# Kernel tuning notes

Hardware: AMD Instinct MI355X
Metric: run time of the kernel (lower is better)

## Reference

```python
import jax, jax.numpy as jnp
import numpy as np

VOCAB = 50257
EMBED = 512
HEADS = 8
HEAD_DIM = EMBED // HEADS
WINDOW = 128
NUM_CLASS = 20
B, S = 4, 2048


def setup_inputs() -> dict:
    key = jax.random.key(0)
    ks = jax.random.split(key, 16)
    sc = 0.02
    inp = {
        'text': jax.random.randint(ks[0], (B, S), 0, VOCAB),
        'emb': jax.random.normal(ks[1], (VOCAB, EMBED), jnp.float32) * sc,
        'in_w': jax.random.normal(ks[2], (3 * EMBED, EMBED), jnp.float32) * sc,
        'in_b': jnp.zeros((3 * EMBED,), jnp.float32),
        'out_w': jax.random.normal(ks[3], (EMBED, EMBED), jnp.float32) * sc,
        'out_b': jnp.zeros((EMBED,), jnp.float32),
        'w1': jax.random.normal(ks[4], (512, EMBED), jnp.float32) * sc,
        'b1': jnp.zeros((512,), jnp.float32),
        'w2': jax.random.normal(ks[5], (256, 512), jnp.float32) * sc,
        'b2': jnp.zeros((256,), jnp.float32),
        'w3': jax.random.normal(ks[6], (128, 256), jnp.float32) * sc,
        'b3': jnp.zeros((128,), jnp.float32),
        'w4': jax.random.normal(ks[7], (NUM_CLASS, 128), jnp.float32) * sc,
        'b4': jnp.zeros((NUM_CLASS,), jnp.float32),
    }
    return inp


def _banded_mask(seq_len, window):
    i = jnp.arange(seq_len)[:, None]
    j = jnp.arange(seq_len)[None, :]
    allowed = jnp.abs(i - j) <= window  # band of width 2*window+1
    return jnp.where(allowed, 0.0, -jnp.inf).astype(jnp.float32)


def reference(text, emb, in_w, in_b, out_w, out_b, w1, b1, w2, b2, w3, b3, w4, b4):
    # Embedding lookup (dropout is identity in eval mode)
    x = emb[text]  # [B, S, E]
    b, s, e = x.shape

    # torch nn.MultiheadAttention: packed in_proj, scaling by 1/sqrt(head_dim)
    wq, wk, wv = in_w[:e], in_w[e:2 * e], in_w[2 * e:]
    bq, bk, bv = in_b[:e], in_b[e:2 * e], in_b[2 * e:]
    q = (x @ wq.T + bq).reshape(b, s, HEADS, HEAD_DIM)
    k = (x @ wk.T + bk).reshape(b, s, HEADS, HEAD_DIM)
    v = (x @ wv.T + bv).reshape(b, s, HEADS, HEAD_DIM)

    mask = _banded_mask(s, WINDOW)  # [S, S] additive, -inf outside band
    scores = jnp.einsum('bihd,bjhd->bhij', q, k) / jnp.sqrt(jnp.float32(HEAD_DIM))
    probs = jax.nn.softmax(scores + mask, axis=-1)  # [B, H, S, S]
    attn = jnp.einsum('bhij,bjhd->bihd', probs, v).reshape(b, s, e)
    attn = attn @ out_w.T + out_b  # [B, S, E]

    # max-pool over sequence
    ctx = jnp.max(attn, axis=1)  # [B, E]

    # MLP head with leaky_relu (negative_slope=0.01, torch default)
    h = jax.nn.leaky_relu(ctx @ w1.T + b1, 0.01)
    h = jax.nn.leaky_relu(h @ w2.T + b2, 0.01)
    h = jax.nn.leaky_relu(h @ w3.T + b3, 0.01)
    return h @ w4.T + b4  # [B, NUM_CLASS]
```

## Files before the change

kernel.cpp:

```cpp
#include <hip/hip_runtime.h>

typedef unsigned short u16;
typedef __attribute__((ext_vector_type(8))) short bf16x8;
typedef __attribute__((ext_vector_type(4))) float f32x4;

#define S_LEN 2048
#define EMBED 512
#define HEADS 8
#define HDIM 64
#define BATCH 4
#define TOKENS (BATCH * S_LEN)

__device__ __forceinline__ u16 f2bf(float f) {
  union { float f; unsigned u; } v;
  v.f = f;
  unsigned r = v.u + 0x7fffu + ((v.u >> 16) & 1u);
  return (u16)(r >> 16);
}

__device__ __forceinline__ void gl2lds16(const void* g, void* l) {
  __builtin_amdgcn_global_load_lds(
      (const __attribute__((address_space(1))) void*)g,
      (__attribute__((address_space(3))) void*)l, 16, 0, 0);
}

__global__ __launch_bounds__(256) void gather_kernel(
    const int* __restrict__ text, const float* __restrict__ emb,
    u16* __restrict__ Xb) {
  const int t = blockIdx.x;
  const int tid = threadIdx.x;
  const size_t src = (size_t)text[t] * EMBED + tid * 2;
  const float2 v = *(const float2*)(emb + src);
  u16* dst = Xb + (size_t)t * EMBED + tid * 2;
  dst[0] = f2bf(v.x);
  dst[1] = f2bf(v.y);
}

__global__ __launch_bounds__(256) void convw_kernel(
    const float* __restrict__ in_w, const float* __restrict__ out_w,
    u16* __restrict__ Wq, u16* __restrict__ Wo) {
  const int idx4 = (blockIdx.x * 256 + threadIdx.x) * 4;
  const float* src;
  u16* dst;
  if (idx4 < 1536 * 512) { src = in_w + idx4; dst = Wq + idx4; }
  else { src = out_w + (idx4 - 1536 * 512); dst = Wo + (idx4 - 1536 * 512); }
  const float4 v = *(const float4*)src;
  dst[0] = f2bf(v.x); dst[1] = f2bf(v.y); dst[2] = f2bf(v.z); dst[3] = f2bf(v.w);
}

__global__ __launch_bounds__(256, 3) void qkv_mfma(
    const u16* __restrict__ Xb, const u16* __restrict__ Wq,
    const float* __restrict__ in_b,
    u16* __restrict__ qg, u16* __restrict__ kg, u16* __restrict__ vt) {
  __shared__ u16 As[128 * 64];
  __shared__ u16 Bs[128 * 64];
  const int m0 = blockIdx.x * 128, n0 = blockIdx.y * 128;
  const int tid = threadIdx.x;
  const int w = tid >> 6, l = tid & 63, quad = l >> 4, ln = l & 15;
  const int rb = (w >> 1) * 64, cb = (w & 1) * 64;

  f32x4 acc[4][4] = {};

  for (int k0 = 0; k0 < EMBED; k0 += 64) {
#pragma unroll
    for (int it = 0; it < 4; ++it) {
      const int chunk = it * 256 + tid;
      const int row = chunk >> 3, cp = chunk & 7, c = cp ^ (row & 7);
      gl2lds16(Xb + (size_t)(m0 + row) * EMBED + k0 + c * 8, &As[chunk * 8]);
      gl2lds16(Wq + (size_t)(n0 + row) * EMBED + k0 + c * 8, &Bs[chunk * 8]);
    }
    __syncthreads();
#pragma unroll
    for (int s = 0; s < 2; ++s) {
      bf16x8 af[4], bf[4];
#pragma unroll
      for (int i = 0; i < 4; ++i) {
        const int r = rb + 16 * i + ln;
        af[i] = *(const bf16x8*)&As[r * 64 + (((s << 2) + quad) ^ (r & 7)) * 8];
      }
#pragma unroll
      for (int j = 0; j < 4; ++j) {
        const int n = cb + 16 * j + ln;
        bf[j] = *(const bf16x8*)&Bs[n * 64 + (((s << 2) + quad) ^ (n & 7)) * 8];
      }
#pragma unroll
      for (int i = 0; i < 4; ++i)
#pragma unroll
        for (int j = 0; j < 4; ++j)
          acc[i][j] = __builtin_amdgcn_mfma_f32_16x16x32_bf16(af[i], bf[j], acc[i][j], 0, 0, 0);
    }
    __syncthreads();
  }

#pragma unroll
  for (int j = 0; j < 4; ++j) {
    const int n = n0 + cb + 16 * j + ln;
    const float bias = in_b[n];
    const int sec = n >> 9, f = n & 511, h = f >> 6, d = f & 63;
#pragma unroll
    for (int i = 0; i < 4; ++i) {
#pragma unroll
      for (int r = 0; r < 4; ++r) {
        const int t = m0 + rb + 16 * i + quad * 4 + r;
        const int b = t >> 11, s = t & 2047;
        const float val = acc[i][j][r] + bias;
        if (sec == 0)
          qg[((size_t)((b * HEADS + h) * S_LEN + s)) * HDIM + d] = f2bf(val * 0.125f);
        else if (sec == 1)
          kg[((size_t)((b * HEADS + h) * S_LEN + s)) * HDIM + d] = f2bf(val);
        else
          vt[((size_t)((b * HEADS + h) * HDIM + d)) * S_LEN + s] = f2bf(val);
      }
    }
  }
}

__global__ __launch_bounds__(256, 3) void attn_mfma(
    const u16* __restrict__ qg, const u16* __restrict__ kg,
    const u16* __restrict__ vt, u16* __restrict__ attnb) {
  __shared__ u16 KV[320 * 64];
  __shared__ u16 Pb[4][16 * 40];
  const int bh = blockIdx.y;
  const int i0 = blockIdx.x * 64;
  const int jb = i0 - 128;
  const int tid = threadIdx.x;
  const int w = tid >> 6, l = tid & 63, quad = l >> 4, ln = l & 15;

  const u16* qrow = qg + ((size_t)bh * S_LEN + i0 + w * 16 + ln) * HDIM;
  bf16x8 qf[2];
  qf[0] = *(const bf16x8*)(qrow + quad * 8);
  qf[1] = *(const bf16x8*)(qrow + 32 + quad * 8);

  const u16* kbase = kg + (size_t)bh * S_LEN * HDIM;
#pragma unroll
  for (int it = 0; it < 10; ++it) {
    const int chunk = it * 256 + tid;
    const int row = chunk >> 3, cp = chunk & 7, c = cp ^ (row & 7);
    int gj = jb + row;
    gj = gj < 0 ? 0 : (gj > S_LEN - 1 ? S_LEN - 1 : gj);
    gl2lds16(kbase + (size_t)gj * HDIM + c * 8, &KV[chunk * 8]);
  }
  __syncthreads();

  f32x4 sc[20];
#pragma unroll
  for (int jt = 0; jt < 20; ++jt) {
    const int r = jt * 16 + ln;
    const bf16x8 b0 = *(const bf16x8*)&KV[r * 64 + ((quad) ^ (r & 7)) * 8];
    const bf16x8 b1 = *(const bf16x8*)&KV[r * 64 + ((4 + quad) ^ (r & 7)) * 8];
    f32x4 a = {};
    a = __builtin_amdgcn_mfma_f32_16x16x32_bf16(qf[0], b0, a, 0, 0, 0);
    a = __builtin_amdgcn_mfma_f32_16x16x32_bf16(qf[1], b1, a, 0, 0, 0);
    sc[jt] = a;
  }
  __syncthreads();

  const u16* vbase = vt + (size_t)bh * HDIM * S_LEN;
#pragma unroll
  for (int it = 0; it < 10; ++it) {
    const int chunk = it * 256 + tid;
    const int row = chunk / 40, cp = chunk % 40, c = cp ^ (row & 7);
    int gc = jb + c * 8;
    gc = gc < 0 ? 0 : (gc > S_LEN - 8 ? S_LEN - 8 : gc);
    gl2lds16(vbase + (size_t)row * S_LEN + gc, &KV[chunk * 8]);
  }

  const int gibase = i0 + w * 16 + quad * 4;
  float mrow[4] = {-1e30f, -1e30f, -1e30f, -1e30f}, lrow[4];
#pragma unroll
  for (int jt = 0; jt < 20; ++jt) {
    const int gj = jb + jt * 16 + ln;
#pragma unroll
    for (int r = 0; r < 4; ++r) {
      const int dij = (gibase + r) - gj;
      const bool valid = (gj >= 0) && (gj < S_LEN) && (dij <= 128) && (dij >= -128);
      const float v = valid ? sc[jt][r] : -1e30f;
      sc[jt][r] = v;
      mrow[r] = fmaxf(mrow[r], v);
    }
  }
#pragma unroll
  for (int r = 0; r < 4; ++r) {
    mrow[r] = fmaxf(mrow[r], __shfl_xor(mrow[r], 1));
    mrow[r] = fmaxf(mrow[r], __shfl_xor(mrow[r], 2));
    mrow[r] = fmaxf(mrow[r], __shfl_xor(mrow[r], 4));
    mrow[r] = fmaxf(mrow[r], __shfl_xor(mrow[r], 8));
    lrow[r] = 0.f;
  }
#pragma unroll
  for (int jt = 0; jt < 20; ++jt)
#pragma unroll
    for (int r = 0; r < 4; ++r) {
      const float e = __expf(sc[jt][r] - mrow[r]);
      sc[jt][r] = e;
      lrow[r] += e;
    }
#pragma unroll
  for (int r = 0; r < 4; ++r) {
    lrow[r] += __shfl_xor(lrow[r], 1);
    lrow[r] += __shfl_xor(lrow[r], 2);
    lrow[r] += __shfl_xor(lrow[r], 4);
    lrow[r] += __shfl_xor(lrow[r], 8);
    lrow[r] = 1.0f / lrow[r];
  }
#pragma unroll
  for (int jt = 0; jt < 20; ++jt)
#pragma unroll
    for (int r = 0; r < 4; ++r) sc[jt][r] *= lrow[r];

  __syncthreads();

  f32x4 oacc[4] = {};
  u16* pb = &Pb[w][0];
#pragma unroll
  for (int kt = 0; kt < 10; ++kt) {
#pragma unroll
    for (int tt = 0; tt < 2; ++tt) {
      const int jt = kt * 2 + tt;
#pragma unroll
      for (int r = 0; r < 4; ++r)
        pb[(quad * 4 + r) * 40 + ln + 16 * tt] = f2bf(sc[jt][r]);
    }
    __asm__ volatile("" ::: "memory");
    const bf16x8 pa = *(const bf16x8*)&pb[ln * 40 + quad * 8];
#pragma unroll
    for (int dt = 0; dt < 4; ++dt) {
      const int d = dt * 16 + ln;
      const bf16x8 vb = *(const bf16x8*)&KV[d * 320 + ((kt * 4 + quad) ^ (d & 7)) * 8];
      oacc[dt] = __builtin_amdgcn_mfma_f32_16x16x32_bf16(pa, vb, oacc[dt], 0, 0, 0);
    }
  }

  const int b = bh >> 3, h = bh & 7;
#pragma unroll
  for (int dt = 0; dt < 4; ++dt) {
    const int d = h * HDIM + dt * 16 + ln;
#pragma unroll
    for (int r = 0; r < 4; ++r) {
      const int gi = i0 + w * 16 + quad * 4 + r;
      attnb[((size_t)(b * S_LEN + gi)) * EMBED + d] = f2bf(oacc[dt][r]);
    }
  }
}

__global__ __launch_bounds__(256, 3) void outproj_mfma(
    const u16* __restrict__ attnb, const u16* __restrict__ Wo,
    const float* __restrict__ out_b, float* __restrict__ pmax) {
  __shared__ u16 As[128 * 64];
  __shared__ u16 Bs[128 * 64];
  __shared__ float red[4][64];
  const int m0 = blockIdx.x * 128, n0 = blockIdx.y * 128;
  const int tid = threadIdx.x;
  const int w = tid >> 6, l = tid & 63, quad = l >> 4, ln = l & 15;
  const int rb = (w >> 1) * 64, cb = (w & 1) * 64;

  f32x4 acc[4][4] = {};

  for (int k0 = 0; k0 < EMBED; k0 += 64) {
#pragma unroll
    for (int it = 0; it < 4; ++it) {
      const int chunk = it * 256 + tid;
      const int row = chunk >> 3, cp = chunk & 7, c = cp ^ (row & 7);
      gl2lds16(attnb + (size_t)(m0 + row) * EMBED + k0 + c * 8, &As[chunk * 8]);
      gl2lds16(Wo + (size_t)(n0 + row) * EMBED + k0 + c * 8, &Bs[chunk * 8]);
    }
    __syncthreads();
#pragma unroll
    for (int s = 0; s < 2; ++s) {
      bf16x8 af[4], bf[4];
#pragma unroll
      for (int i = 0; i < 4; ++i) {
        const int r = rb + 16 * i + ln;
        af[i] = *(const bf16x8*)&As[r * 64 + (((s << 2) + quad) ^ (r & 7)) * 8];
      }
#pragma unroll
      for (int j = 0; j < 4; ++j) {
        const int n = cb + 16 * j + ln;
        bf[j] = *(const bf16x8*)&Bs[n * 64 + (((s << 2) + quad) ^ (n & 7)) * 8];
      }
#pragma unroll
      for (int i = 0; i < 4; ++i)
#pragma unroll
        for (int j = 0; j < 4; ++j)
          acc[i][j] = __builtin_amdgcn_mfma_f32_16x16x32_bf16(af[i], bf[j], acc[i][j], 0, 0, 0);
    }
    __syncthreads();
  }

  float cm[4];
#pragma unroll
  for (int j = 0; j < 4; ++j) {
    float m = -1e30f;
#pragma unroll
    for (int i = 0; i < 4; ++i)
#pragma unroll
      for (int r = 0; r < 4; ++r) m = fmaxf(m, acc[i][j][r]);
    m = fmaxf(m, __shfl_xor(m, 16));
    m = fmaxf(m, __shfl_xor(m, 32));
    cm[j] = m;
  }
  if (l < 16) {
#pragma unroll
    for (int j = 0; j < 4; ++j) red[w][ln + 16 * j] = cm[j];
  }
  __syncthreads();
  if (tid < 128) {
    const int ch = tid >> 6, cw = tid & 63;
    const float m = fmaxf(red[ch][cw], red[ch + 2][cw]);
    const int n = n0 + ch * 64 + cw;
    const int b = m0 >> 11, stile = (m0 >> 7) & 15;
    pmax[(size_t)(b * 16 + stile) * EMBED + n] = m + out_b[n];
  }
}

__global__ __launch_bounds__(256) void mlp_ctx_l1(
    const float* __restrict__ pmax, const float* __restrict__ w1,
    const float* __restrict__ b1, float* __restrict__ h1g) {
  __shared__ float ctx[512];
  const int b = blockIdx.x >> 3, chunk = blockIdx.x & 7;
  const int tid = threadIdx.x;

  for (int e = tid; e < 512; e += 256) {
    float m = -1e30f;
#pragma unroll
    for (int t = 0; t < 16; ++t) m = fmaxf(m, pmax[(size_t)(b * 16 + t) * 512 + e]);
    ctx[e] = m;
  }
  __syncthreads();

  const int o = chunk * 64 + (tid >> 2), kq = tid & 3;
  float acc = 0.f;
  const float* wr = w1 + (size_t)o * 512 + kq * 128;
  const float* xr = ctx + kq * 128;
  for (int k = 0; k < 128; k += 4) {
    const float4 wv = *(const float4*)(wr + k);
    const float4 xv = *(const float4*)(xr + k);
    acc += wv.x * xv.x + wv.y * xv.y + wv.z * xv.z + wv.w * xv.w;
  }
  acc += __shfl_xor(acc, 1);
  acc += __shfl_xor(acc, 2);
  if (kq == 0) {
    const float a = acc + b1[o];
    h1g[b * 512 + o] = a > 0.f ? a : 0.01f * a;
  }
}

__global__ __launch_bounds__(256) void mlp_l2(
    const float* __restrict__ h1g, const float* __restrict__ w2,
    const float* __restrict__ b2, float* __restrict__ h2g) {
  __shared__ float xb[512];
  const int b = blockIdx.x >> 2, chunk = blockIdx.x & 3;
  const int tid = threadIdx.x;
  for (int e = tid; e < 512; e += 256) xb[e] = h1g[b * 512 + e];
  __syncthreads();

  const int o = chunk * 64 + (tid >> 2), kq = tid & 3;
  float acc = 0.f;
  const float* wr = w2 + (size_t)o * 512 + kq * 128;
  const float* xr = xb + kq * 128;
  for (int k = 0; k < 128; k += 4) {
    const float4 wv = *(const float4*)(wr + k);
    const float4 xv = *(const float4*)(xr + k);
    acc += wv.x * xv.x + wv.y * xv.y + wv.z * xv.z + wv.w * xv.w;
  }
  acc += __shfl_xor(acc, 1);
  acc += __shfl_xor(acc, 2);
  if (kq == 0) {
    const float a = acc + b2[o];
    h2g[b * 256 + o] = a > 0.f ? a : 0.01f * a;
  }
}

__global__ __launch_bounds__(256) void mlp_l34(
    const float* __restrict__ h2g,
    const float* __restrict__ w3, const float* __restrict__ b3,
    const float* __restrict__ w4, const float* __restrict__ b4,
    float* __restrict__ out) {
  __shared__ float xb[256], h3[128];
  const int b = blockIdx.x, tid = threadIdx.x;
  if (tid < 256) xb[tid] = h2g[b * 256 + tid];
  __syncthreads();

  {
    const int o = tid >> 1, kh = tid & 1;
    float acc = 0.f;
    const float* wr = w3 + (size_t)o * 256 + kh * 128;
    const float* xr = xb + kh * 128;
    for (int k = 0; k < 128; k += 4) {
      const float4 wv = *(const float4*)(wr + k);
      const float4 xv = *(const float4*)(xr + k);
      acc += wv.x * xv.x + wv.y * xv.y + wv.z * xv.z + wv.w * xv.w;
    }
    acc += __shfl_xor(acc, 1);
    if (kh == 0) { const float a = acc + b3[o]; h3[o] = a > 0.f ? a : 0.01f * a; }
  }
  __syncthreads();

  if (tid < 160) {
    const int o = tid >> 3, ks = tid & 7;
    const float* wr = w4 + (size_t)o * 128 + ks * 16;
    const float* xr = h3 + ks * 16;
    float acc = 0.f;
    for (int k = 0; k < 16; k += 4) {
      const float4 wv = *(const float4*)(wr + k);
      const float4 xv = *(const float4*)(xr + k);
      acc += wv.x * xv.x + wv.y * xv.y + wv.z * xv.z + wv.w * xv.w;
    }
    acc += __shfl_xor(acc, 1);
    acc += __shfl_xor(acc, 2);
    acc += __shfl_xor(acc, 4);
    if (ks == 0) out[b * 20 + o] = acc + b4[o];
  }
}

extern "C" void kernel_launch(void* const* d_in, const int* in_sizes, int n_in,
                              void* d_out, int out_size, void* d_ws, size_t ws_size,
                              hipStream_t stream) {
  (void)in_sizes; (void)n_in; (void)out_size; (void)ws_size;
  const int*   text  = (const int*)d_in[0];
  const float* emb   = (const float*)d_in[1];
  const float* in_w  = (const float*)d_in[2];
  const float* in_b  = (const float*)d_in[3];
  const float* out_w = (const float*)d_in[4];
  const float* out_b = (const float*)d_in[5];
  const float* w1 = (const float*)d_in[6];
  const float* b1 = (const float*)d_in[7];
  const float* w2 = (const float*)d_in[8];
  const float* b2 = (const float*)d_in[9];
  const float* w3 = (const float*)d_in[10];
  const float* b3 = (const float*)d_in[11];
  const float* w4 = (const float*)d_in[12];
  const float* b4 = (const float*)d_in[13];

  char* ws = (char*)d_ws;
  u16* Xb   = (u16*)(ws);
  u16* Wq   = (u16*)(ws + 8388608);
  u16* Wo   = (u16*)(ws + 9961472);
  u16* qg   = (u16*)(ws + 10485760);
  u16* kg   = (u16*)(ws + 18874368);
  u16* vt   = (u16*)(ws + 27262976);
  u16* attn = (u16*)(ws + 35651584);
  float* pmax = (float*)(ws + 44040192);
  float* h1g  = (float*)(ws + 44171264);
  float* h2g  = (float*)(ws + 44179456);

  gather_kernel<<<TOKENS, 256, 0, stream>>>(text, emb, Xb);
  convw_kernel<<<1024, 256, 0, stream>>>(in_w, out_w, Wq, Wo);
  qkv_mfma<<<dim3(64, 12), 256, 0, stream>>>(Xb, Wq, in_b, qg, kg, vt);
  attn_mfma<<<dim3(32, 32), 256, 0, stream>>>(qg, kg, vt, attn);
  outproj_mfma<<<dim3(64, 4), 256, 0, stream>>>(attn, Wo, out_b, pmax);
  mlp_ctx_l1<<<32, 256, 0, stream>>>(pmax, w1, b1, h1g);
  mlp_l2<<<16, 256, 0, stream>>>(h1g, w2, b2, h2g);
  mlp_l34<<<4, 256, 0, stream>>>(h2g, w3, b3, w4, b4, (float*)d_out);
}
```

Measured before the change: 240.5 us.

## Fuse prep kernels, skip out-of-band attention tiles, swap grid order, pack stores

Merges the embedding gather and the weight bf16 conversion into one kernel that uses 8-wide vector loads and stores. In the attention kernel, each wave now computes only the key tiles that overlap its band, skipping the rest in the QK, softmax and PV loops. P is staged through a full swizzled LDS buffer instead of a per-wave bounce buffer, which doubles LDS use and lowers launch bounds to 2 blocks per CU. GEMM grids are transposed so consecutive blocks share the same row tile, and V-transpose stores are packed in pairs.

```diff
diff --git a/kernel.cpp b/kernel.cpp
--- a/kernel.cpp
+++ b/kernel.cpp
@@ -24,28 +24,31 @@
       (__attribute__((address_space(3))) void*)l, 16, 0, 0);
 }
 
-__global__ __launch_bounds__(256) void gather_kernel(
+__global__ __launch_bounds__(256) void prep_kernel(
     const int* __restrict__ text, const float* __restrict__ emb,
-    u16* __restrict__ Xb) {
-  const int t = blockIdx.x;
-  const int tid = threadIdx.x;
-  const size_t src = (size_t)text[t] * EMBED + tid * 2;
-  const float2 v = *(const float2*)(emb + src);
-  u16* dst = Xb + (size_t)t * EMBED + tid * 2;
-  dst[0] = f2bf(v.x);
-  dst[1] = f2bf(v.y);
-}
-
-__global__ __launch_bounds__(256) void convw_kernel(
     const float* __restrict__ in_w, const float* __restrict__ out_w,
-    u16* __restrict__ Wq, u16* __restrict__ Wo) {
-  const int idx4 = (blockIdx.x * 256 + threadIdx.x) * 4;
+    u16* __restrict__ Xb, u16* __restrict__ Wq, u16* __restrict__ Wo) {
+  const int bid = blockIdx.x;
+  const int idx = bid * 256 + threadIdx.x;
   const float* src;
   u16* dst;
-  if (idx4 < 1536 * 512) { src = in_w + idx4; dst = Wq + idx4; }
-  else { src = out_w + (idx4 - 1536 * 512); dst = Wo + (idx4 - 1536 * 512); }
-  const float4 v = *(const float4*)src;
-  dst[0] = f2bf(v.x); dst[1] = f2bf(v.y); dst[2] = f2bf(v.z); dst[3] = f2bf(v.w);
+  if (bid < 2048) {
+    const int t = idx >> 6, c8 = (idx & 63) * 8;
+    src = emb + (size_t)text[t] * EMBED + c8;
+    dst = Xb + (size_t)t * EMBED + c8;
+  } else {
+    const int w8 = (idx - 2048 * 256) * 8;
+    if (w8 < 1536 * 512) { src = in_w + w8; dst = Wq + w8; }
+    else { src = out_w + (w8 - 1536 * 512); dst = Wo + (w8 - 1536 * 512); }
+  }
+  const float4 a = *(const float4*)src;
+  const float4 b = *(const float4*)(src + 4);
+  uint4 p;
+  p.x = (unsigned)f2bf(a.x) | ((unsigned)f2bf(a.y) << 16);
+  p.y = (unsigned)f2bf(a.z) | ((unsigned)f2bf(a.w) << 16);
+  p.z = (unsigned)f2bf(b.x) | ((unsigned)f2bf(b.y) << 16);
+  p.w = (unsigned)f2bf(b.z) | ((unsigned)f2bf(b.w) << 16);
+  *(uint4*)dst = p;
 }
 
 __global__ __launch_bounds__(256, 3) void qkv_mfma(
@@ -54,7 +57,7 @@
     u16* __restrict__ qg, u16* __restrict__ kg, u16* __restrict__ vt) {
   __shared__ u16 As[128 * 64];
   __shared__ u16 Bs[128 * 64];
-  const int m0 = blockIdx.x * 128, n0 = blockIdx.y * 128;
+  const int m0 = blockIdx.y * 128, n0 = blockIdx.x * 128;
   const int tid = threadIdx.x;
   const int w = tid >> 6, l = tid & 63, quad = l >> 4, ln = l & 15;
   const int rb = (w >> 1) * 64, cb = (w & 1) * 64;
@@ -99,32 +102,47 @@
     const int sec = n >> 9, f = n & 511, h = f >> 6, d = f & 63;
 #pragma unroll
     for (int i = 0; i < 4; ++i) {
-#pragma unroll
-      for (int r = 0; r < 4; ++r) {
-        const int t = m0 + rb + 16 * i + quad * 4 + r;
-        const int b = t >> 11, s = t & 2047;
-        const float val = acc[i][j][r] + bias;
-        if (sec == 0)
-          qg[((size_t)((b * HEADS + h) * S_LEN + s)) * HDIM + d] = f2bf(val * 0.125f);
-        else if (sec == 1)
-          kg[((size_t)((b * HEADS + h) * S_LEN + s)) * HDIM + d] = f2bf(val);
-        else
-          vt[((size_t)((b * HEADS + h) * HDIM + d)) * S_LEN + s] = f2bf(val);
+      if (sec == 2) {
+#pragma unroll
+        for (int r = 0; r < 4; r += 2) {
+          const int t = m0 + rb + 16 * i + quad * 4 + r;
+          const int b = t >> 11, s = t & 2047;
+          const unsigned p = (unsigned)f2bf(acc[i][j][r] + bias) |
+                             ((unsigned)f2bf(acc[i][j][r + 1] + bias) << 16);
+          *(unsigned*)&vt[((size_t)((b * HEADS + h) * HDIM + d)) * S_LEN + s] = p;
+        }
+      } else {
+#pragma unroll
+        for (int r = 0; r < 4; ++r) {
+          const int t = m0 + rb + 16 * i + quad * 4 + r;
+          const int b = t >> 11, s = t & 2047;
+          const float val = acc[i][j][r] + bias;
+          if (sec == 0)
+            qg[((size_t)((b * HEADS + h) * S_LEN + s)) * HDIM + d] = f2bf(val * 0.125f);
+          else
+            kg[((size_t)((b * HEADS + h) * S_LEN + s)) * HDIM + d] = f2bf(val);
+        }
       }
     }
   }
 }
 
-__global__ __launch_bounds__(256, 3) void attn_mfma(
+__global__ __launch_bounds__(256, 2) void attn_mfma(
     const u16* __restrict__ qg, const u16* __restrict__ kg,
     const u16* __restrict__ vt, u16* __restrict__ attnb) {
   __shared__ u16 KV[320 * 64];
-  __shared__ u16 Pb[4][16 * 40];
+  __shared__ u16 Ps[64 * 320];
   const int bh = blockIdx.y;
   const int i0 = blockIdx.x * 64;
   const int jb = i0 - 128;
   const int tid = threadIdx.x;
   const int w = tid >> 6, l = tid & 63, quad = l >> 4, ln = l & 15;
+
+  const int clo = (w * 16 > -jb) ? w * 16 : -jb;
+  const int chiraw = w * 16 + 271, chimax = 2047 - jb;
+  const int chi = chiraw < chimax ? chiraw : chimax;
+  const int kt0 = clo >> 5, kt1 = chi >> 5;
+  const int jt0 = kt0 << 1, jt1 = (kt1 << 1) + 1;
 
   const u16* qrow = qg + ((size_t)bh * S_LEN + i0 + w * 16 + ln) * HDIM;
   bf16x8 qf[2];
@@ -145,6 +163,7 @@
   f32x4 sc[20];
 #pragma unroll
   for (int jt = 0; jt < 20; ++jt) {
+    if (jt < jt0 || jt > jt1) continue;
     const int r = jt * 16 + ln;
     const bf16x8 b0 = *(const bf16x8*)&KV[r * 64 + ((quad) ^ (r & 7)) * 8];
     const bf16x8 b1 = *(const bf16x8*)&KV[r * 64 + ((4 + quad) ^ (r & 7)) * 8];
@@ -169,6 +188,7 @@
   float mrow[4] = {-1e30f, -1e30f, -1e30f, -1e30f}, lrow[4];
 #pragma unroll
   for (int jt = 0; jt < 20; ++jt) {
+    if (jt < jt0 || jt > jt1) continue;
     const int gj = jb + jt * 16 + ln;
 #pragma unroll
     for (int r = 0; r < 4; ++r) {
@@ -188,13 +208,15 @@
     lrow[r] = 0.f;
   }
 #pragma unroll
-  for (int jt = 0; jt < 20; ++jt)
+  for (int jt = 0; jt < 20; ++jt) {
+    if (jt < jt0 || jt > jt1) continue;
 #pragma unroll
     for (int r = 0; r < 4; ++r) {
       const float e = __expf(sc[jt][r] - mrow[r]);
       sc[jt][r] = e;
       lrow[r] += e;
     }
+  }
 #pragma unroll
   for (int r = 0; r < 4; ++r) {
     lrow[r] += __shfl_xor(lrow[r], 1);
@@ -203,30 +225,31 @@
     lrow[r] += __shfl_xor(lrow[r], 8);
     lrow[r] = 1.0f / lrow[r];
   }
-#pragma unroll
-  for (int jt = 0; jt < 20; ++jt)
-#pragma unroll
-    for (int r = 0; r < 4; ++r) sc[jt][r] *= lrow[r];
-
+
+#pragma unroll
+  for (int jt = 0; jt < 20; ++jt) {
+    if (jt < jt0 || jt > jt1) continue;
+    const int cchunk = jt * 2 + (ln >> 3);
+#pragma unroll
+    for (int r = 0; r < 4; ++r) {
+      const int m = quad * 4 + r;
+      const int swz = cchunk ^ (m & 7);
+      Ps[(w * 16 + m) * 320 + swz * 8 + (ln & 7)] = f2bf(sc[jt][r] * lrow[r]);
+    }
+  }
   __syncthreads();
 
   f32x4 oacc[4] = {};
-  u16* pb = &Pb[w][0];
+  const int prow = w * 16 + ln;
 #pragma unroll
   for (int kt = 0; kt < 10; ++kt) {
-#pragma unroll
-    for (int tt = 0; tt < 2; ++tt) {
-      const int jt = kt * 2 + tt;
-#pragma unroll
-      for (int r = 0; r < 4; ++r)
-        pb[(quad * 4 + r) * 40 + ln + 16 * tt] = f2bf(sc[jt][r]);
-    }
-    __asm__ volatile("" ::: "memory");
-    const bf16x8 pa = *(const bf16x8*)&pb[ln * 40 + quad * 8];
+    if (kt < kt0 || kt > kt1) continue;
+    const int c = kt * 4 + quad;
+    const bf16x8 pa = *(const bf16x8*)&Ps[prow * 320 + (c ^ (ln & 7)) * 8];
 #pragma unroll
     for (int dt = 0; dt < 4; ++dt) {
       const int d = dt * 16 + ln;
-      const bf16x8 vb = *(const bf16x8*)&KV[d * 320 + ((kt * 4 + quad) ^ (d & 7)) * 8];
+      const bf16x8 vb = *(const bf16x8*)&KV[d * 320 + (c ^ (d & 7)) * 8];
       oacc[dt] = __builtin_amdgcn_mfma_f32_16x16x32_bf16(pa, vb, oacc[dt], 0, 0, 0);
     }
   }
@@ -249,7 +272,7 @@
   __shared__ u16 As[128 * 64];
   __shared__ u16 Bs[128 * 64];
   __shared__ float red[4][64];
-  const int m0 = blockIdx.x * 128, n0 = blockIdx.y * 128;
+  const int m0 = blockIdx.y * 128, n0 = blockIdx.x * 128;
   const int tid = threadIdx.x;
   const int w = tid >> 6, l = tid & 63, quad = l >> 4, ln = l & 15;
   const int rb = (w >> 1) * 64, cb = (w & 1) * 64;
@@ -444,11 +467,10 @@
   float* h1g  = (float*)(ws + 44171264);
   float* h2g  = (float*)(ws + 44179456);
 
-  gather_kernel<<<TOKENS, 256, 0, stream>>>(text, emb, Xb);
-  convw_kernel<<<1024, 256, 0, stream>>>(in_w, out_w, Wq, Wo);
-  qkv_mfma<<<dim3(64, 12), 256, 0, stream>>>(Xb, Wq, in_b, qg, kg, vt);
+  prep_kernel<<<2560, 256, 0, stream>>>(text, emb, in_w, out_w, Xb, Wq, Wo);
+  qkv_mfma<<<dim3(12, 64), 256, 0, stream>>>(Xb, Wq, in_b, qg, kg, vt);
   attn_mfma<<<dim3(32, 32), 256, 0, stream>>>(qg, kg, vt, attn);
-  outproj_mfma<<<dim3(64, 4), 256, 0, stream>>>(attn, Wo, out_b, pmax);
+  outproj_mfma<<<dim3(4, 64), 256, 0, stream>>>(attn, Wo, out_b, pmax);
   mlp_ctx_l1<<<32, 256, 0, stream>>>(pmax, w1, b1, h1g);
   mlp_l2<<<16, 256, 0, stream>>>(h1g, w2, b2, h2g);
   mlp_l34<<<4, 256, 0, stream>>>(h2g, w3, b3, w4, b4, (float*)d_out);
```

Result: no change. 243.5 us (+1.3%).
